# Performance work log

Hardware: AMD Instinct MI355X
Metric: run time of the kernel (lower is better)

## Reference

```python
import jax, jax.numpy as jnp
import numpy as np

EPS_LN = 1e-5

def layer_norm(x, w, b):
    u = x.mean(-1, keepdims=True)
    s = jnp.mean((x - u) ** 2, -1, keepdims=True)
    return w * ((x - u) / jnp.sqrt(s + EPS_LN)) + b

def mlp(x, W, b, lw, lb):
    return jax.nn.relu(layer_norm(x @ W + b, lw, lb))

def mlp_gate(x, W, b, lw, lb):
    return jax.nn.sigmoid(layer_norm(x @ W + b, lw, lb))

def setup_inputs() -> dict:
    N, D = 768, 64
    key = jax.random.key(0)
    ks = jax.random.split(key, 12)
    inp = {
        'corr_index': jax.random.normal(ks[0], (N, N, 2), jnp.float32),
        'nei_index': jax.random.randint(ks[1], (N, N), 0, 2).astype(jnp.int64),
        'nei_num': jax.random.randint(ks[2], (N,), 0, N).astype(jnp.int64),
        'hidden_state': jax.random.normal(ks[3], (N, D), jnp.float32),
        'agent_v': jax.random.normal(ks[4], (N, 2), jnp.float32),
        # relativeLayer: MLP(3, D)
        'rel_w': jax.random.normal(ks[5], (3, D), jnp.float32) * (1.0 / np.sqrt(3)),
        'rel_b': jnp.zeros((D,), jnp.float32),
        'rel_lw': jnp.ones((D,), jnp.float32),
        'rel_lb': jnp.zeros((D,), jnp.float32),
        # ngate: MLP_gate(3D, D)
        'ng_w': jax.random.normal(ks[6], (3 * D, D), jnp.float32) * (1.0 / np.sqrt(3 * D)),
        'ng_b': jnp.zeros((D,), jnp.float32),
        'ng_lw': jnp.ones((D,), jnp.float32),
        'ng_lb': jnp.zeros((D,), jnp.float32),
        # WAr: MLP(3D, 1) -- LayerNorm(1) is identity in the source
        'war_w': jax.random.normal(ks[7], (3 * D, 1), jnp.float32) * (1.0 / np.sqrt(3 * D)),
        'war_b': jnp.zeros((1,), jnp.float32),
        # weight: MLP(D, D)
        'wt_w': jax.random.normal(ks[8], (D, D), jnp.float32) * (1.0 / np.sqrt(D)),
        'wt_b': jnp.zeros((D,), jnp.float32),
        'wt_lw': jnp.ones((D,), jnp.float32),
        'wt_lb': jnp.zeros((D,), jnp.float32),
    }
    return inp

def reference(corr_index, nei_index, nei_num, hidden_state, agent_v,
              rel_w, rel_b, rel_lw, rel_lb,
              ng_w, ng_b, ng_lw, ng_lb,
              war_w, war_b,
              wt_w, wt_b, wt_lw, wt_lb):
    N, D = hidden_state.shape
    # pair layout: row i*N+j  (i = receiver row of the NxN grid, j = column)
    agent_vt = jnp.tile(agent_v, (N, 1))                     # [N*N, 2], row i*N+j -> agent_v[j]
    corr_t = corr_index.reshape(N * N, 2)
    dot = agent_vt[:, 0] * corr_t[:, 0] + agent_vt[:, 1] * corr_t[:, 1]
    judge = jnp.sum(agent_vt ** 2, -1)
    angle = dot / (jnp.sqrt(judge * jnp.sum(corr_t ** 2, -1)) + 1e-10)
    angle = jnp.where(judge == 0, -1.0, angle)
    corr3 = jnp.concatenate([corr_t, angle[:, None]], -1)    # [N*N, 3]

    r_t = mlp(corr3, rel_w, rel_b, rel_lw, rel_lb)           # [N*N, D]
    nei_inputs = jnp.tile(hidden_state, (N, 1))              # row i*N+j -> h[j]
    hi_t = jnp.repeat(hidden_state, N, axis=0)               # row i*N+j -> h[i]
    tmp = jnp.concatenate([r_t, hi_t, nei_inputs], 1)        # [N*N, 3D]

    mask = (nei_index.reshape(N * N) > 0)
    nGate = mlp_gate(tmp, ng_w, ng_b, ng_lw, ng_lb)          # [N*N, D]
    tt = jax.nn.relu(tmp @ war_w + war_b).reshape(-1)        # LayerNorm(1) == identity

    Pos = jnp.where(mask, tt, 0.0).reshape(N, N)
    Pos = jnp.where(Pos == 0, -10000.0, Pos)
    Pos = jax.nn.softmax(Pos, axis=1)
    Pos_t = Pos.reshape(-1)

    H = jnp.where(mask[:, None], nei_inputs * nGate * Pos_t[:, None], 0.0)
    H_sum = mlp(H.reshape(N, N, D).sum(1), wt_w, wt_b, wt_lw, wt_lb)
    return hidden_state + H_sum
```

## Files before the change

### kernel.cpp

```cpp
#include <hip/hip_runtime.h>
#include <math.h>

#define NN 768
#define DD 64
#define WPB 4
#define TPW (NN / 16 / WPB)
#define RSTRIDE 34
#define PREBLKS 18

typedef _Float16 half8 __attribute__((ext_vector_type(8)));
typedef float    f32x4 __attribute__((ext_vector_type(4)));
typedef __fp16   p2f   __attribute__((ext_vector_type(2)));

union FragU { uint4 u4; unsigned int u[4]; half8 h; };
union PkU   { unsigned int u; p2f p; };

__device__ __forceinline__ unsigned int pk2(float a, float b) {
    PkU t; t.p = __builtin_amdgcn_cvt_pkrtz(a, b); return t.u;
}
__device__ __forceinline__ float lane_bcast(float v, int src) {
    return __int_as_float(__builtin_amdgcn_readlane(__float_as_int(v), src));
}
__device__ __forceinline__ f32x4 mfma16(FragU a, FragU b, f32x4 c) {
    return __builtin_amdgcn_mfma_f32_16x16x32_f16(a.h, b.h, c, 0, 0, 0);
}

__global__ __launch_bounds__(256) void k_prepack(
    const float* __restrict__ hs, const float* __restrict__ ng_w,
    const float* __restrict__ ng_b, const float* __restrict__ war_w,
    const float* __restrict__ war_b,
    const float* __restrict__ rel_w, const float* __restrict__ rel_b,
    const float* __restrict__ rel_lw, const float* __restrict__ rel_lb,
    float* __restrict__ sbase, float* __restrict__ warb, float* __restrict__ war3,
    unsigned int* __restrict__ hf16,
    unsigned int* __restrict__ afragS, unsigned int* __restrict__ afragR,
    float* __restrict__ mom)
{
    const int t = threadIdx.x, blk = blockIdx.x;
    const int lane = t & 63, q = t >> 6, g = lane >> 4, c16 = lane & 15;

    if (blk >= PREBLKS) {
        const int row = (blk - PREBLKS) * 4 + q;
        const float hv = hs[row * DD + lane];
        float a2 = ng_b[lane];
        #pragma unroll 8
        for (int k = 0; k < DD; ++k)
            a2 = fmaf(lane_bcast(hv, k), ng_w[(DD + k) * DD + lane], a2);
        sbase[row * DD + lane] = a2;
        float t2 = hv * war_w[DD + lane];
        float t3 = hv * war_w[2 * DD + lane];
        #pragma unroll
        for (int o = 32; o; o >>= 1) { t2 += __shfl_xor(t2, o); t3 += __shfl_xor(t3, o); }
        if (lane == 0) { warb[row] = t2 + war_b[0]; war3[row] = t3; }
        return;
    }

    for (int idx = blk * 256 + t; idx < NN * 32; idx += PREBLKS * 256) {
        const int row = idx >> 5, c = idx & 31;
        hf16[idx] = pk2(hs[row * DD + 2 * c], hs[row * DD + 2 * c + 1]);
    }

    if (blk < 16) {
        const int b = blk >> 2, c = blk & 3;
        const int dout = 16 * b + c16;
        const int k0 = 32 * c + g * 8 + 2 * q;
        const int r0 = (k0 < 64) ? k0 : (k0 + 64);
        afragS[(blk * 64 + lane) * 4 + q] =
            pk2(ng_w[r0 * DD + dout], ng_w[(r0 + 1) * DD + dout]);
    } else if (blk == 16) {
        const int b = q;
        const int d = 16 * b + c16;
        const float rlwd = rel_lw[d], rlbd = rel_lb[d];
        const float c0 = rel_w[d] * rlwd;
        const float c1 = rel_w[DD + d] * rlwd;
        const float c2 = rel_w[2 * DD + d] * rlwd;
        const float c3 = rel_b[d] * rlwd;
        PkU h01, h23, h45;
        h01.p = __builtin_amdgcn_cvt_pkrtz(c0, c1);
        h23.p = __builtin_amdgcn_cvt_pkrtz(c2, c3);
        h45.p = __builtin_amdgcn_cvt_pkrtz(rlwd, rlbd);
        const unsigned l01 = pk2(c0 - (float)h01.p[0], c1 - (float)h01.p[1]);
        const unsigned l23 = pk2(c2 - (float)h23.p[0], c3 - (float)h23.p[1]);
        const unsigned l45 = pk2(rlwd - (float)h45.p[0], rlbd - (float)h45.p[1]);
        const unsigned int base = (b * 64 + lane) * 4;
        unsigned v0, v1, v2;
        if (g == 0 || g == 1)      { v0 = h01.u; v1 = h23.u; v2 = h45.u; }
        else if (g == 2)           { v0 = l01;   v1 = l23;   v2 = l45;   }
        else                       { v0 = 0u;    v1 = 0u;    v2 = 0u;    }
        afragR[base + 0] = v0;
        afragR[base + 1] = v1;
        afragR[base + 2] = v2;
        afragR[base + 3] = 0u;
    } else {
        if (t < 64) {
            const float x0 = rel_w[t], x1 = rel_w[DD + t], x2 = rel_w[2 * DD + t];
            const float x3 = rel_b[t];
            float v[14] = {x0, x1, x2, x3,
                           x0 * x0, x1 * x1, x2 * x2, x3 * x3,
                           x0 * x1, x0 * x2, x0 * x3, x1 * x2, x1 * x3, x2 * x3};
            #pragma unroll
            for (int qq = 0; qq < 14; ++qq) {
                float s = v[qq];
                #pragma unroll
                for (int o = 32; o; o >>= 1) s += __shfl_xor(s, o);
                if (t == 0) mom[qq] = s * (1.f / 64.f);
            }
        }
    }
}

__global__ __launch_bounds__(64 * WPB) void k_main(
    const float* __restrict__ corr, const int* __restrict__ nei,
    const float* __restrict__ hs, const float* __restrict__ av,
    const float* __restrict__ ng_lw, const float* __restrict__ ng_lb,
    const float* __restrict__ war_w,
    const float* __restrict__ sbase, const float* __restrict__ warb,
    const float* __restrict__ war3,
    const unsigned int* __restrict__ afragS, const unsigned int* __restrict__ afragR,
    const unsigned int* __restrict__ hf16, const float* __restrict__ mom,
    const float* __restrict__ wt_w, const float* __restrict__ wt_b,
    const float* __restrict__ wt_lw, const float* __restrict__ wt_lb,
    float* __restrict__ out)
{
    const int i = blockIdx.x;
    const int tid = threadIdx.x;
    const int lane = tid & 63, wave = tid >> 6;
    const int g = lane >> 4, c16 = lane & 15;

    __shared__ unsigned int smr[WPB * 16 * RSTRIDE];
    __shared__ float sm_red[WPB][DD];
    __shared__ float sm_m[WPB], sm_l[WPB];

    FragU aS[4][4], aR[4];
    #pragma unroll
    for (int b = 0; b < 4; ++b)
        #pragma unroll
        for (int c = 0; c < 4; ++c)
            aS[b][c].u4 = ((const uint4*)afragS)[(b * 4 + c) * 64 + lane];
    #pragma unroll
    for (int b = 0; b < 4; ++b) aR[b].u4 = ((const uint4*)afragR)[b * 64 + lane];

    float sb[16], nlwv[16], nlbv[16], wv16[16];
    #pragma unroll
    for (int b = 0; b < 4; ++b)
        #pragma unroll
        for (int r = 0; r < 4; ++r) {
            const int dout = 16 * b + g * 4 + r;
            sb[b * 4 + r]   = sbase[i * DD + dout];
            nlwv[b * 4 + r] = ng_lw[dout];
            nlbv[b * 4 + r] = ng_lb[dout];
            wv16[b * 4 + r] = war_w[dout];
        }

    const float m0 = mom[0], m1 = mom[1], m2 = mom[2], m3 = mom[3];
    const float M00 = mom[4], M11 = mom[5], M22 = mom[6], M33 = mom[7];
    const float M01 = mom[8], M02 = mom[9], M03 = mom[10];
    const float M12 = mom[11], M13 = mom[12], M23 = mom[13];

    const float warbase = warb[i];
    unsigned int* wrbase = smr + (wave * 16 + c16) * RSTRIDE;

    float acc[16];
    #pragma unroll
    for (int x = 0; x < 16; ++x) acc[x] = 0.f;
    float mrun = -INFINITY, lrun = 0.f;

    int jj = 16 * wave + c16;
    float2 cc = ((const float2*)corr)[i * NN + jj];
    float2 vv = ((const float2*)av)[jj];
    int    nv = nei[i * NN + jj];
    float  w3 = war3[jj];
    FragU bx2, bx3;
    bx2.u4 = *(const uint4*)(hf16 + jj * 32 + 4 * g);
    bx3.u4 = *(const uint4*)(hf16 + jj * 32 + 16 + 4 * g);

    #pragma unroll 1
    for (int t = 0; t < TPW; ++t) {
        const f32x4 hv0 = *(const f32x4*)(hs + jj * DD +  0 + 4 * g);
        const f32x4 hv1 = *(const f32x4*)(hs + jj * DD + 16 + 4 * g);
        const f32x4 hv2 = *(const f32x4*)(hs + jj * DD + 32 + 4 * g);
        const f32x4 hv3 = *(const f32x4*)(hs + jj * DD + 48 + 4 * g);

        const int tn  = (t + 1 < TPW) ? (t + 1) : t;
        const int jjn = 16 * (wave + WPB * tn) + c16;
        const float2 cc_n = ((const float2*)corr)[i * NN + jjn];
        const float2 vv_n = ((const float2*)av)[jjn];
        const int    nv_n = nei[i * NN + jjn];
        const float  w3_n = war3[jjn];
        FragU bx2_n, bx3_n;
        bx2_n.u4 = *(const uint4*)(hf16 + jjn * 32 + 4 * g);
        bx3_n.u4 = *(const uint4*)(hf16 + jjn * 32 + 16 + 4 * g);

        const float cx = cc.x, cy = cc.y;
        const float judge = vv.x * vv.x + vv.y * vv.y;
        const float dotv = fmaf(vv.x, cx, vv.y * cy);
        const float cn = cx * cx + cy * cy;
        float angle = __fdividef(dotv, sqrtf(judge * cn) + 1e-10f);
        if (judge == 0.f) angle = -1.f;

        const float u = fmaf(cx, m0, fmaf(cy, m1, fmaf(angle, m2, m3)));
        float e2 = M33;
        e2 = fmaf(cx * cx, M00, e2);
        e2 = fmaf(cy * cy, M11, e2);
        e2 = fmaf(angle * angle, M22, e2);
        e2 = fmaf(2.f * cx, fmaf(cy, M01, fmaf(angle, M02, M03)), e2);
        e2 = fmaf(2.f * cy, fmaf(angle, M12, M13), e2);
        e2 = fmaf(2.f * angle, M23, e2);
        const float vare = (e2 - u * u) + 1e-5f;
        const float inv = rsqrtf(vare);
        const float sig = vare * inv;

        PkU s01, s23, s45;
        s01.p = __builtin_amdgcn_cvt_pkrtz(cx, cy);
        s23.p = __builtin_amdgcn_cvt_pkrtz(angle, 1.f);
        s45.p = __builtin_amdgcn_cvt_pkrtz(-u, sig);
        const unsigned l0 = pk2(cx - (float)s01.p[0], cy - (float)s01.p[1]);
        const unsigned l1 = pk2(angle - (float)s23.p[0], 0.f);
        const unsigned l2 = pk2((-u) - (float)s45.p[0], sig - (float)s45.p[1]);
        FragU b1;
        b1.u[0] = (g == 3) ? 0u : ((g == 1) ? l0 : s01.u);
        b1.u[1] = (g == 3) ? 0u : ((g == 1) ? l1 : s23.u);
        b1.u[2] = (g == 3) ? 0u : ((g == 1) ? l2 : s45.u);
        b1.u[3] = 0u;

        const f32x4 Z = {0.f, 0.f, 0.f, 0.f};
        float wd = 0.f;
        #pragma unroll
        for (int b = 0; b < 4; ++b) {
            const f32x4 P = mfma16(aR[b], b1, Z);
            const float r0f = fmaxf(P[0], 0.f) * inv;
            const float r1f = fmaxf(P[1], 0.f) * inv;
            const float r2f = fmaxf(P[2], 0.f) * inv;
            const float r3f = fmaxf(P[3], 0.f) * inv;
            wd = fmaf(r0f, wv16[b * 4 + 0], wd);
            wd = fmaf(r1f, wv16[b * 4 + 1], wd);
            wd = fmaf(r2f, wv16[b * 4 + 2], wd);
            wd = fmaf(r3f, wv16[b * 4 + 3], wd);
            uint2 wv;
            wv.x = pk2(r0f, r1f);
            wv.y = pk2(r2f, r3f);
            *(uint2*)(wrbase + 8 * b + 2 * g) = wv;
        }
        wd += __shfl_xor(wd, 16);
        wd += __shfl_xor(wd, 32);

        FragU bx0, bx1;
        {
            const uint2 lo0 = *(const uint2*)(wrbase + 4 * g);
            const uint2 hi0 = *(const uint2*)(wrbase + 4 * g + 2);
            bx0.u[0] = lo0.x; bx0.u[1] = lo0.y; bx0.u[2] = hi0.x; bx0.u[3] = hi0.y;
            const uint2 lo1 = *(const uint2*)(wrbase + 16 + 4 * g);
            const uint2 hi1 = *(const uint2*)(wrbase + 16 + 4 * g + 2);
            bx1.u[0] = lo1.x; bx1.u[1] = lo1.y; bx1.u[2] = hi1.x; bx1.u[3] = hi1.y;
        }

        f32x4 S[4];
        #pragma unroll
        for (int b = 0; b < 4; ++b) {
            f32x4 cinit = {sb[b * 4 + 0], sb[b * 4 + 1], sb[b * 4 + 2], sb[b * 4 + 3]};
            cinit = mfma16(aS[b][0], bx0, cinit);
            cinit = mfma16(aS[b][1], bx1, cinit);
            cinit = mfma16(aS[b][2], bx2, cinit);
            cinit = mfma16(aS[b][3], bx3, cinit);
            S[b] = cinit;
        }

        float s1 = 0.f, s2 = 0.f;
        #pragma unroll
        for (int x = 0; x < 16; ++x) {
            const float sv = S[x >> 2][x & 3];
            s1 += sv; s2 = fmaf(sv, sv, s2);
        }
        s1 += __shfl_xor(s1, 16); s1 += __shfl_xor(s1, 32);
        s2 += __shfl_xor(s2, 16); s2 += __shfl_xor(s2, 32);
        const float u2 = s1 * (1.f / 64.f);
        const float var2 = fmaf(s2, 1.f / 64.f, -u2 * u2);
        const float inv2 = rsqrtf(var2 + 1e-5f);

        float tt = wd + w3 + warbase;
        tt = fmaxf(tt, 0.f);
        const bool msk = nv > 0;
        const float p = (msk && tt > 0.f) ? tt : -10000.f;

        float pm = p;
        pm = fmaxf(pm, __shfl_xor(pm, 1));
        pm = fmaxf(pm, __shfl_xor(pm, 2));
        pm = fmaxf(pm, __shfl_xor(pm, 4));
        pm = fmaxf(pm, __shfl_xor(pm, 8));
        const float mn = fmaxf(mrun, pm);
        const float alpha = __expf(mrun - mn);
        const float e = __expf(p - mn);
        const float eacc = msk ? e : 0.f;
        lrun = fmaf(lrun, alpha, e);
        mrun = mn;

        #pragma unroll
        for (int b = 0; b < 4; ++b) {
            const f32x4 hvb = (b == 0) ? hv0 : (b == 1) ? hv1 : (b == 2) ? hv2 : hv3;
            #pragma unroll
            for (int r = 0; r < 4; ++r) {
                const float ngv = fmaf((S[b][r] - u2) * inv2, nlwv[b * 4 + r],
                                       nlbv[b * 4 + r]);
                const float gate = __fdividef(1.f, 1.f + __expf(-ngv));
                acc[b * 4 + r] = fmaf(acc[b * 4 + r], alpha, eacc * gate * hvb[r]);
            }
        }

        jj = jjn; cc = cc_n; vv = vv_n; nv = nv_n; w3 = w3_n;
        bx2 = bx2_n; bx3 = bx3_n;
    }

    #pragma unroll
    for (int o = 1; o <= 8; o <<= 1) {
        lrun += __shfl_xor(lrun, o);
        #pragma unroll
        for (int x = 0; x < 16; ++x) acc[x] += __shfl_xor(acc[x], o);
    }
    if (c16 == 0) {
        #pragma unroll
        for (int b = 0; b < 4; ++b)
            #pragma unroll
            for (int r = 0; r < 4; ++r)
                sm_red[wave][16 * b + g * 4 + r] = acc[b * 4 + r];
        if (lane == 0) { sm_m[wave] = mrun; sm_l[wave] = lrun; }
    }
    __syncthreads();

    if (tid < DD) {
        float M = sm_m[0];
        #pragma unroll
        for (int w = 1; w < WPB; ++w) M = fmaxf(M, sm_m[w]);
        float L = 0.f, A = 0.f;
        #pragma unroll
        for (int w = 0; w < WPB; ++w) {
            const float f = __expf(sm_m[w] - M);
            L = fmaf(sm_l[w], f, L);
            A = fmaf(sm_red[w][tid], f, A);
        }
        const float Hv = A / L;
        float v = wt_b[tid];
        #pragma unroll 8
        for (int k = 0; k < DD; ++k)
            v = fmaf(lane_bcast(Hv, k), wt_w[k * DD + tid], v);
        float t1 = v, t2 = v * v;
        #pragma unroll
        for (int o = 32; o; o >>= 1) { t1 += __shfl_xor(t1, o); t2 += __shfl_xor(t2, o); }
        const float uo = t1 * (1.f / 64.f);
        const float varo = fmaf(t2, 1.f / 64.f, -uo * uo);
        const float invo = rsqrtf(varo + 1e-5f);
        const float ro = fmaf((v - uo) * invo, wt_lw[tid], wt_lb[tid]);
        out[i * DD + tid] = hs[i * DD + tid] + fmaxf(ro, 0.f);
    }
}

extern "C" void kernel_launch(void* const* d_in, const int* in_sizes, int n_in,
                              void* d_out, int out_size, void* d_ws, size_t ws_size,
                              hipStream_t stream) {
    const float* corr   = (const float*)d_in[0];
    const int*   nei    = (const int*)  d_in[1];
    const float* hs     = (const float*)d_in[3];
    const float* av     = (const float*)d_in[4];
    const float* rel_w  = (const float*)d_in[5];
    const float* rel_b  = (const float*)d_in[6];
    const float* rel_lw = (const float*)d_in[7];
    const float* rel_lb = (const float*)d_in[8];
    const float* ng_w   = (const float*)d_in[9];
    const float* ng_b   = (const float*)d_in[10];
    const float* ng_lw  = (const float*)d_in[11];
    const float* ng_lb  = (const float*)d_in[12];
    const float* war_w  = (const float*)d_in[13];
    const float* war_b  = (const float*)d_in[14];
    const float* wt_w   = (const float*)d_in[15];
    const float* wt_b   = (const float*)d_in[16];
    const float* wt_lw  = (const float*)d_in[17];
    const float* wt_lb  = (const float*)d_in[18];
    float* out = (float*)d_out;

    float* ws    = (float*)d_ws;
    float* sbase = ws;
    float* warb  = sbase + NN * DD;
    float* war3  = warb + NN;
    float* mom   = war3 + NN;
    unsigned int* hf16   = (unsigned int*)(mom + 16);
    unsigned int* afragS = hf16 + NN * 32;
    unsigned int* afragR = afragS + 16 * 64 * 4;

    k_prepack<<<PREBLKS + NN / 4, 256, 0, stream>>>(
        hs, ng_w, ng_b, war_w, war_b, rel_w, rel_b, rel_lw, rel_lb,
        sbase, warb, war3, hf16, afragS, afragR, mom);
    k_main<<<NN, 64 * WPB, 0, stream>>>(
        corr, nei, hs, av, ng_lw, ng_lb, war_w, sbase, warb, war3,
        afragS, afragR, hf16, mom, wt_w, wt_b, wt_lw, wt_lb, out);
}
```

Measured before the change: 146.7 us.

## Fuse prepack kernel into main kernel, computing weights and bases per block

```diff
diff --git a/kernel.cpp b/kernel.cpp
--- a/kernel.cpp
+++ b/kernel.cpp
@@ -6,7 +6,6 @@
 #define WPB 4
 #define TPW (NN / 16 / WPB)
 #define RSTRIDE 34
-#define PREBLKS 18
 
 typedef _Float16 half8 __attribute__((ext_vector_type(8)));
 typedef float    f32x4 __attribute__((ext_vector_type(4)));
@@ -21,54 +20,50 @@
 __device__ __forceinline__ float lane_bcast(float v, int src) {
     return __int_as_float(__builtin_amdgcn_readlane(__float_as_int(v), src));
 }
+__device__ __forceinline__ float rfl(float v) {
+    return __int_as_float(__builtin_amdgcn_readfirstlane(__float_as_int(v)));
+}
 __device__ __forceinline__ f32x4 mfma16(FragU a, FragU b, f32x4 c) {
     return __builtin_amdgcn_mfma_f32_16x16x32_f16(a.h, b.h, c, 0, 0, 0);
 }
 
-__global__ __launch_bounds__(256) void k_prepack(
-    const float* __restrict__ hs, const float* __restrict__ ng_w,
-    const float* __restrict__ ng_b, const float* __restrict__ war_w,
-    const float* __restrict__ war_b,
+__global__ __launch_bounds__(64 * WPB) void k_main(
+    const float* __restrict__ corr, const int* __restrict__ nei,
+    const float* __restrict__ hs, const float* __restrict__ av,
     const float* __restrict__ rel_w, const float* __restrict__ rel_b,
     const float* __restrict__ rel_lw, const float* __restrict__ rel_lb,
-    float* __restrict__ sbase, float* __restrict__ warb, float* __restrict__ war3,
-    unsigned int* __restrict__ hf16,
-    unsigned int* __restrict__ afragS, unsigned int* __restrict__ afragR,
-    float* __restrict__ mom)
+    const float* __restrict__ ng_w, const float* __restrict__ ng_b,
+    const float* __restrict__ ng_lw, const float* __restrict__ ng_lb,
+    const float* __restrict__ war_w, const float* __restrict__ war_b,
+    const float* __restrict__ wt_w, const float* __restrict__ wt_b,
+    const float* __restrict__ wt_lw, const float* __restrict__ wt_lb,
+    float* __restrict__ out)
 {
-    const int t = threadIdx.x, blk = blockIdx.x;
-    const int lane = t & 63, q = t >> 6, g = lane >> 4, c16 = lane & 15;
-
-    if (blk >= PREBLKS) {
-        const int row = (blk - PREBLKS) * 4 + q;
-        const float hv = hs[row * DD + lane];
-        float a2 = ng_b[lane];
-        #pragma unroll 8
-        for (int k = 0; k < DD; ++k)
-            a2 = fmaf(lane_bcast(hv, k), ng_w[(DD + k) * DD + lane], a2);
-        sbase[row * DD + lane] = a2;
-        float t2 = hv * war_w[DD + lane];
-        float t3 = hv * war_w[2 * DD + lane];
-        #pragma unroll
-        for (int o = 32; o; o >>= 1) { t2 += __shfl_xor(t2, o); t3 += __shfl_xor(t3, o); }
-        if (lane == 0) { warb[row] = t2 + war_b[0]; war3[row] = t3; }
-        return;
-    }
-
-    for (int idx = blk * 256 + t; idx < NN * 32; idx += PREBLKS * 256) {
-        const int row = idx >> 5, c = idx & 31;
-        hf16[idx] = pk2(hs[row * DD + 2 * c], hs[row * DD + 2 * c + 1]);
-    }
-
-    if (blk < 16) {
-        const int b = blk >> 2, c = blk & 3;
+    const int i = blockIdx.x;
+    const int tid = threadIdx.x;
+    const int lane = tid & 63, wave = tid >> 6;
+    const int g = lane >> 4, c16 = lane & 15;
+
+    __shared__ unsigned int smr[WPB * 16 * RSTRIDE];
+    __shared__ float sm_red[WPB][DD];
+    __shared__ float sm_m[WPB], sm_l[WPB];
+
+    FragU aS[4][4], aR[4];
+    #pragma unroll
+    for (int b = 0; b < 4; ++b) {
         const int dout = 16 * b + c16;
-        const int k0 = 32 * c + g * 8 + 2 * q;
-        const int r0 = (k0 < 64) ? k0 : (k0 + 64);
-        afragS[(blk * 64 + lane) * 4 + q] =
-            pk2(ng_w[r0 * DD + dout], ng_w[(r0 + 1) * DD + dout]);
-    } else if (blk == 16) {
-        const int b = q;
+        #pragma unroll
+        for (int c = 0; c < 4; ++c)
+            #pragma unroll
+            for (int q = 0; q < 4; ++q) {
+                const int k0 = 32 * c + g * 8 + 2 * q;
+                const int r0 = (k0 < 64) ? k0 : (k0 + 64);
+                aS[b][c].u[q] =
+                    pk2(ng_w[r0 * DD + dout], ng_w[(r0 + 1) * DD + dout]);
+            }
+    }
+    #pragma unroll
+    for (int b = 0; b < 4; ++b) {
         const int d = 16 * b + c16;
         const float rlwd = rel_lw[d], rlbd = rel_lb[d];
         const float c0 = rel_w[d] * rlwd;
@@ -79,85 +74,68 @@
         h01.p = __builtin_amdgcn_cvt_pkrtz(c0, c1);
         h23.p = __builtin_amdgcn_cvt_pkrtz(c2, c3);
         h45.p = __builtin_amdgcn_cvt_pkrtz(rlwd, rlbd);
-        const unsigned l01 = pk2(c0 - (float)h01.p[0], c1 - (float)h01.p[1]);
-        const unsigned l23 = pk2(c2 - (float)h23.p[0], c3 - (float)h23.p[1]);
-        const unsigned l45 = pk2(rlwd - (float)h45.p[0], rlbd - (float)h45.p[1]);
-        const unsigned int base = (b * 64 + lane) * 4;
         unsigned v0, v1, v2;
-        if (g == 0 || g == 1)      { v0 = h01.u; v1 = h23.u; v2 = h45.u; }
-        else if (g == 2)           { v0 = l01;   v1 = l23;   v2 = l45;   }
-        else                       { v0 = 0u;    v1 = 0u;    v2 = 0u;    }
-        afragR[base + 0] = v0;
-        afragR[base + 1] = v1;
-        afragR[base + 2] = v2;
-        afragR[base + 3] = 0u;
-    } else {
-        if (t < 64) {
-            const float x0 = rel_w[t], x1 = rel_w[DD + t], x2 = rel_w[2 * DD + t];
-            const float x3 = rel_b[t];
-            float v[14] = {x0, x1, x2, x3,
-                           x0 * x0, x1 * x1, x2 * x2, x3 * x3,
-                           x0 * x1, x0 * x2, x0 * x3, x1 * x2, x1 * x3, x2 * x3};
-            #pragma unroll
-            for (int qq = 0; qq < 14; ++qq) {
-                float s = v[qq];
-                #pragma unroll
-                for (int o = 32; o; o >>= 1) s += __shfl_xor(s, o);
-                if (t == 0) mom[qq] = s * (1.f / 64.f);
-            }
-        }
-    }
-}
-
-__global__ __launch_bounds__(64 * WPB) void k_main(
-    const float* __restrict__ corr, const int* __restrict__ nei,
-    const float* __restrict__ hs, const float* __restrict__ av,
-    const float* __restrict__ ng_lw, const float* __restrict__ ng_lb,
-    const float* __restrict__ war_w,
-    const float* __restrict__ sbase, const float* __restrict__ warb,
-    const float* __restrict__ war3,
-    const unsigned int* __restrict__ afragS, const unsigned int* __restrict__ afragR,
-    const unsigned int* __restrict__ hf16, const float* __restrict__ mom,
-    const float* __restrict__ wt_w, const float* __restrict__ wt_b,
-    const float* __restrict__ wt_lw, const float* __restrict__ wt_lb,
-    float* __restrict__ out)
-{
-    const int i = blockIdx.x;
-    const int tid = threadIdx.x;
-    const int lane = tid & 63, wave = tid >> 6;
-    const int g = lane >> 4, c16 = lane & 15;
-
-    __shared__ unsigned int smr[WPB * 16 * RSTRIDE];
-    __shared__ float sm_red[WPB][DD];
-    __shared__ float sm_m[WPB], sm_l[WPB];
-
-    FragU aS[4][4], aR[4];
-    #pragma unroll
-    for (int b = 0; b < 4; ++b)
-        #pragma unroll
-        for (int c = 0; c < 4; ++c)
-            aS[b][c].u4 = ((const uint4*)afragS)[(b * 4 + c) * 64 + lane];
-    #pragma unroll
-    for (int b = 0; b < 4; ++b) aR[b].u4 = ((const uint4*)afragR)[b * 64 + lane];
-
-    float sb[16], nlwv[16], nlbv[16], wv16[16];
-    #pragma unroll
-    for (int b = 0; b < 4; ++b)
+        if (g == 0 || g == 1) { v0 = h01.u; v1 = h23.u; v2 = h45.u; }
+        else if (g == 2) {
+            v0 = pk2(c0 - (float)h01.p[0], c1 - (float)h01.p[1]);
+            v1 = pk2(c2 - (float)h23.p[0], c3 - (float)h23.p[1]);
+            v2 = pk2(rlwd - (float)h45.p[0], rlbd - (float)h45.p[1]);
+        } else { v0 = 0u; v1 = 0u; v2 = 0u; }
+        aR[b].u[0] = v0; aR[b].u[1] = v1; aR[b].u[2] = v2; aR[b].u[3] = 0u;
+    }
+    float mv[14];
+    {
+        const float x0 = rel_w[lane], x1 = rel_w[DD + lane];
+        const float x2 = rel_w[2 * DD + lane], x3 = rel_b[lane];
+        mv[0] = x0; mv[1] = x1; mv[2] = x2; mv[3] = x3;
+        mv[4] = x0 * x0; mv[5] = x1 * x1; mv[6] = x2 * x2; mv[7] = x3 * x3;
+        mv[8] = x0 * x1; mv[9] = x0 * x2; mv[10] = x0 * x3;
+        mv[11] = x1 * x2; mv[12] = x1 * x3; mv[13] = x2 * x3;
+        #pragma unroll
+        for (int q = 0; q < 14; ++q) {
+            float s = mv[q];
+            #pragma unroll
+            for (int o = 32; o; o >>= 1) s += __shfl_xor(s, o);
+            mv[q] = rfl(s * (1.f / 64.f));
+        }
+    }
+    const float m0 = mv[0], m1 = mv[1], m2 = mv[2], m3 = mv[3];
+    const float M00 = mv[4], M11 = mv[5], M22 = mv[6], M33 = mv[7];
+    const float M01 = mv[8], M02 = mv[9], M03 = mv[10];
+    const float M12 = mv[11], M13 = mv[12], M23 = mv[13];
+
+    {
+        const float hvi = hs[i * DD + lane];
+        float a2 = ng_b[lane];
+        #pragma unroll 8
+        for (int k = 0; k < DD; ++k)
+            a2 = fmaf(lane_bcast(hvi, k), ng_w[(DD + k) * DD + lane], a2);
+        sm_red[wave][lane] = a2;
+    }
+    float warbase;
+    {
+        const float hvi = hs[i * DD + lane];
+        float t2 = hvi * war_w[DD + lane];
+        #pragma unroll
+        for (int o = 32; o; o >>= 1) t2 += __shfl_xor(t2, o);
+        warbase = rfl(t2) + war_b[0];
+    }
+
+    float sb[16], nlwv[16], nlbv[16], wv16[16], wv3[16];
+    #pragma unroll
+    for (int b = 0; b < 4; ++b) {
+        const f32x4 sbv = *(const f32x4*)(&sm_red[wave][16 * b + 4 * g]);
         #pragma unroll
         for (int r = 0; r < 4; ++r) {
-            const int dout = 16 * b + g * 4 + r;
-            sb[b * 4 + r]   = sbase[i * DD + dout];
+            const int dout = 16 * b + 4 * g + r;
+            sb[b * 4 + r]   = sbv[r];
             nlwv[b * 4 + r] = ng_lw[dout];
             nlbv[b * 4 + r] = ng_lb[dout];
             wv16[b * 4 + r] = war_w[dout];
-        }
-
-    const float m0 = mom[0], m1 = mom[1], m2 = mom[2], m3 = mom[3];
-    const float M00 = mom[4], M11 = mom[5], M22 = mom[6], M33 = mom[7];
-    const float M01 = mom[8], M02 = mom[9], M03 = mom[10];
-    const float M12 = mom[11], M13 = mom[12], M23 = mom[13];
-
-    const float warbase = warb[i];
+            wv3[b * 4 + r]  = war_w[2 * DD + dout];
+        }
+    }
+
     unsigned int* wrbase = smr + (wave * 16 + c16) * RSTRIDE;
 
     float acc[16];
@@ -169,10 +147,17 @@
     float2 cc = ((const float2*)corr)[i * NN + jj];
     float2 vv = ((const float2*)av)[jj];
     int    nv = nei[i * NN + jj];
-    float  w3 = war3[jj];
     FragU bx2, bx3;
-    bx2.u4 = *(const uint4*)(hf16 + jj * 32 + 4 * g);
-    bx3.u4 = *(const uint4*)(hf16 + jj * 32 + 16 + 4 * g);
+    {
+        const f32x4 pA = *(const f32x4*)(hs + jj * DD + 8 * g);
+        const f32x4 pB = *(const f32x4*)(hs + jj * DD + 8 * g + 4);
+        const f32x4 pC = *(const f32x4*)(hs + jj * DD + 32 + 8 * g);
+        const f32x4 pD = *(const f32x4*)(hs + jj * DD + 32 + 8 * g + 4);
+        bx2.u[0] = pk2(pA[0], pA[1]); bx2.u[1] = pk2(pA[2], pA[3]);
+        bx2.u[2] = pk2(pB[0], pB[1]); bx2.u[3] = pk2(pB[2], pB[3]);
+        bx3.u[0] = pk2(pC[0], pC[1]); bx3.u[1] = pk2(pC[2], pC[3]);
+        bx3.u[2] = pk2(pD[0], pD[1]); bx3.u[3] = pk2(pD[2], pD[3]);
+    }
 
     #pragma unroll 1
     for (int t = 0; t < TPW; ++t) {
@@ -186,10 +171,17 @@
         const float2 cc_n = ((const float2*)corr)[i * NN + jjn];
         const float2 vv_n = ((const float2*)av)[jjn];
         const int    nv_n = nei[i * NN + jjn];
-        const float  w3_n = war3[jjn];
         FragU bx2_n, bx3_n;
-        bx2_n.u4 = *(const uint4*)(hf16 + jjn * 32 + 4 * g);
-        bx3_n.u4 = *(const uint4*)(hf16 + jjn * 32 + 16 + 4 * g);
+        {
+            const f32x4 pA = *(const f32x4*)(hs + jjn * DD + 8 * g);
+            const f32x4 pB = *(const f32x4*)(hs + jjn * DD + 8 * g + 4);
+            const f32x4 pC = *(const f32x4*)(hs + jjn * DD + 32 + 8 * g);
+            const f32x4 pD = *(const f32x4*)(hs + jjn * DD + 32 + 8 * g + 4);
+            bx2_n.u[0] = pk2(pA[0], pA[1]); bx2_n.u[1] = pk2(pA[2], pA[3]);
+            bx2_n.u[2] = pk2(pB[0], pB[1]); bx2_n.u[3] = pk2(pB[2], pB[3]);
+            bx3_n.u[0] = pk2(pC[0], pC[1]); bx3_n.u[1] = pk2(pC[2], pC[3]);
+            bx3_n.u[2] = pk2(pD[0], pD[1]); bx3_n.u[3] = pk2(pD[2], pD[3]);
+        }
 
         const float cx = cc.x, cy = cc.y;
         const float judge = vv.x * vv.x + vv.y * vv.y;
@@ -241,6 +233,12 @@
             wv.y = pk2(r2f, r3f);
             *(uint2*)(wrbase + 8 * b + 2 * g) = wv;
         }
+        #pragma unroll
+        for (int b = 0; b < 4; ++b) {
+            const f32x4 hvb = (b == 0) ? hv0 : (b == 1) ? hv1 : (b == 2) ? hv2 : hv3;
+            #pragma unroll
+            for (int r = 0; r < 4; ++r) wd = fmaf(hvb[r], wv3[b * 4 + r], wd);
+        }
         wd += __shfl_xor(wd, 16);
         wd += __shfl_xor(wd, 32);
 
@@ -277,7 +275,7 @@
         const float var2 = fmaf(s2, 1.f / 64.f, -u2 * u2);
         const float inv2 = rsqrtf(var2 + 1e-5f);
 
-        float tt = wd + w3 + warbase;
+        float tt = wd + warbase;
         tt = fmaxf(tt, 0.f);
         const bool msk = nv > 0;
         const float p = (msk && tt > 0.f) ? tt : -10000.f;
@@ -306,7 +304,7 @@
             }
         }
 
-        jj = jjn; cc = cc_n; vv = vv_n; nv = nv_n; w3 = w3_n;
+        jj = jjn; cc = cc_n; vv = vv_n; nv = nv_n;
         bx2 = bx2_n; bx3 = bx3_n;
     }
 
@@ -316,6 +314,7 @@
         #pragma unroll
         for (int x = 0; x < 16; ++x) acc[x] += __shfl_xor(acc[x], o);
     }
+    __syncthreads();
     if (c16 == 0) {
         #pragma unroll
         for (int b = 0; b < 4; ++b)
@@ -376,19 +375,8 @@
     const float* wt_lb  = (const float*)d_in[18];
     float* out = (float*)d_out;
 
-    float* ws    = (float*)d_ws;
-    float* sbase = ws;
-    float* warb  = sbase + NN * DD;
-    float* war3  = warb + NN;
-    float* mom   = war3 + NN;
-    unsigned int* hf16   = (unsigned int*)(mom + 16);
-    unsigned int* afragS = hf16 + NN * 32;
-    unsigned int* afragR = afragS + 16 * 64 * 4;
-
-    k_prepack<<<PREBLKS + NN / 4, 256, 0, stream>>>(
-        hs, ng_w, ng_b, war_w, war_b, rel_w, rel_b, rel_lw, rel_lb,
-        sbase, warb, war3, hf16, afragS, afragR, mom);
     k_main<<<NN, 64 * WPB, 0, stream>>>(
-        corr, nei, hs, av, ng_lw, ng_lb, war_w, sbase, warb, war3,
-        afragS, afragR, hf16, mom, wt_w, wt_b, wt_lw, wt_lb, out);
-}
+        corr, nei, hs, av, rel_w, rel_b, rel_lw, rel_lb,
+        ng_w, ng_b, ng_lw, ng_lb, war_w, war_b,
+        wt_w, wt_b, wt_lw, wt_lb, out);
+}
```

Result: slower. 187.3 us (+27.6%).
